# Kernel tuning notes

Hardware: AMD Instinct MI355X
Metric: run time of the kernel (lower is better)

The kernel has to match this reference:

```python
import jax, jax.numpy as jnp
import numpy as np

TEMPERATURE = 0.07
COS_EPS = 1e-8          # torch F.cosine_similarity eps
MASK_FILL = -9e15       # value used to mask the diagonal


def setup_inputs() -> dict:
    key = jax.random.key(0)
    k1, k2 = jax.random.split(key)
    B, D = 4096, 256
    z_i = jax.random.normal(k1, (B, D), dtype=jnp.float32)
    z_j = jax.random.normal(k2, (B, D), dtype=jnp.float32)
    return {"z_i": z_i, "z_j": z_j}


def reference(z_i, z_j):
    B = z_i.shape[0]
    z = jnp.concatenate([z_i, z_j], axis=0)                 # [2B, D]
    # cosine similarity = normalized-GEMM (same math as broadcasted version)
    norms = jnp.maximum(jnp.linalg.norm(z, axis=-1, keepdims=True), COS_EPS)
    zn = z / norms                                          # [2B, D]
    sim = zn @ zn.T                                         # [2B, 2B]
    # fused diagonal mask + temperature scale
    diag = jnp.eye(2 * B, dtype=bool)
    logits = jnp.where(diag, MASK_FILL, sim) / TEMPERATURE  # [2B, 2B]
    # positive pair labels: row k pairs with row (k+B) mod 2B
    labels = jnp.concatenate([jnp.arange(B, 2 * B), jnp.arange(0, B)])
    logp = jax.nn.log_softmax(logits, axis=-1)
    loss = -jnp.mean(jnp.take_along_axis(logp, labels[:, None], axis=-1))
    return loss
```

## Files before the change

### kernel.cpp

```cpp
#include <hip/hip_runtime.h>
#include <hip/hip_bf16.h>

#define B_ROWS 4096
#define TWOB   8192
#define DIM    256
#define INV_T  14.285714285714286f

#define BM 128
#define BN 128
#define NSTRIP 8
#define CT_PER_STRIP 8

typedef __bf16 bf16x8 __attribute__((ext_vector_type(8)));
typedef float  f32x4  __attribute__((ext_vector_type(4)));

__global__ __launch_bounds__(256) void normalize_k(const float* __restrict__ zi,
                                                   const float* __restrict__ zj,
                                                   unsigned short* __restrict__ zn,
                                                   float* __restrict__ loss_acc,
                                                   unsigned int* __restrict__ counter) {
    if (blockIdx.x == 0 && threadIdx.x == 0) {
        loss_acc[0] = 0.0f;
        counter[0]  = 0u;
    }
    int wave = threadIdx.x >> 6;
    int lane = threadIdx.x & 63;
    int row  = blockIdx.x * 4 + wave;
    const float* src = (row < B_ROWS) ? (zi + (size_t)row * DIM)
                                      : (zj + (size_t)(row - B_ROWS) * DIM);
    float4 v = reinterpret_cast<const float4*>(src)[lane];
    float ss = v.x * v.x + v.y * v.y + v.z * v.z + v.w * v.w;
#pragma unroll
    for (int off = 32; off >= 1; off >>= 1) ss += __shfl_xor(ss, off);
    float norm = sqrtf(ss);
    norm = fmaxf(norm, 1e-8f);
    float inv = 1.0f / norm;
    ushort4 o;
    o.x = __builtin_bit_cast(unsigned short, __float2bfloat16(v.x * inv));
    o.y = __builtin_bit_cast(unsigned short, __float2bfloat16(v.y * inv));
    o.z = __builtin_bit_cast(unsigned short, __float2bfloat16(v.z * inv));
    o.w = __builtin_bit_cast(unsigned short, __float2bfloat16(v.w * inv));
    reinterpret_cast<ushort4*>(zn)[(size_t)row * 64 + lane] = o;
}

__global__ __launch_bounds__(256) void ntxent_main(const unsigned short* __restrict__ znu,
                                                   float* __restrict__ pos,
                                                   float* __restrict__ strip_sums) {
    const __bf16* zn = (const __bf16*)znu;
    __shared__ __attribute__((aligned(16))) __bf16 As[8][BM * 32];
    __shared__ __attribute__((aligned(16))) __bf16 Bs[2][BN * 32];

    const int tid  = threadIdx.x;
    const int wave = tid >> 6;
    const int lane = tid & 63;
    const int wr = wave >> 1, wc = wave & 1;
    const int quad = lane >> 4, lc = lane & 15;
    const int rt    = blockIdx.x;
    const int strip = blockIdx.y;
    const int row0  = rt * BM;
    const int posTile = (rt + 32) & 63;

    int stg_off[2];
#pragma unroll
    for (int t = 0; t < 2; ++t) {
        int c  = (wave * 2 + t) * 64 + lane;
        int m  = c >> 2;
        int kc = (c & 3) ^ ((m & 3) ^ ((m >> 2) & 3));
        stg_off[t] = m * DIM + kc * 8;
    }

    const int sw    = (lc & 3) ^ ((lc >> 2) & 3);
    const int aBase = (wr * 64 + lc) * 64 + ((quad ^ sw) * 16);
    const int bBase = (wc * 64 + lc) * 64 + ((quad ^ sw) * 16);

#pragma unroll
    for (int kt = 0; kt < 8; ++kt) {
#pragma unroll
        for (int t = 0; t < 2; ++t) {
            const int j = wave * 2 + t;
            const __bf16* ga = zn + row0 * DIM + kt * 32 + stg_off[t];
            __builtin_amdgcn_global_load_lds(
                (const __attribute__((address_space(1))) void*)ga,
                (__attribute__((address_space(3))) void*)((char*)As + kt * 8192 + j * 1024), 16, 0, 0);
        }
    }
    {
        const int col0 = strip * CT_PER_STRIP * BN;
#pragma unroll
        for (int t = 0; t < 2; ++t) {
            const int j = wave * 2 + t;
            const __bf16* gb = zn + col0 * DIM + stg_off[t];
            __builtin_amdgcn_global_load_lds(
                (const __attribute__((address_space(1))) void*)gb,
                (__attribute__((address_space(3))) void*)((char*)Bs + j * 1024), 16, 0, 0);
        }
    }

    f32x4 acc[4][4];
    float rsum[4][4];
#pragma unroll
    for (int mi = 0; mi < 4; ++mi)
#pragma unroll
        for (int r = 0; r < 4; ++r) rsum[mi][r] = 0.0f;

    for (int ct = 0; ct < CT_PER_STRIP; ++ct) {
        const int colTile = strip * CT_PER_STRIP + ct;
        const int col0 = colTile * BN;
#pragma unroll
        for (int mi = 0; mi < 4; ++mi)
#pragma unroll
            for (int ni = 0; ni < 4; ++ni) acc[mi][ni] = f32x4{0.f, 0.f, 0.f, 0.f};

#pragma unroll
        for (int kt = 0; kt < 8; ++kt) {
            __syncthreads();

            {
                const int nct = (kt == 7) ? ct + 1 : ct;
                const int nkt = (kt + 1) & 7;
                if (nct < CT_PER_STRIP) {
                    const int ncol0 = (strip * CT_PER_STRIP + nct) * BN;
#pragma unroll
                    for (int t = 0; t < 2; ++t) {
                        const int j = wave * 2 + t;
                        const __bf16* gb = zn + ncol0 * DIM + nkt * 32 + stg_off[t];
                        __builtin_amdgcn_global_load_lds(
                            (const __attribute__((address_space(1))) void*)gb,
                            (__attribute__((address_space(3))) void*)((char*)Bs + ((kt + 1) & 1) * 8192 + j * 1024),
                            16, 0, 0);
                    }
                }
            }

            bf16x8 af[4], bfr[4];
#pragma unroll
            for (int mi = 0; mi < 4; ++mi)
                af[mi] = *(const bf16x8*)((const char*)As + kt * 8192 + aBase + mi * 1024);
#pragma unroll
            for (int ni = 0; ni < 4; ++ni)
                bfr[ni] = *(const bf16x8*)((const char*)Bs + (kt & 1) * 8192 + bBase + ni * 1024);
#pragma unroll
            for (int mi = 0; mi < 4; ++mi)
#pragma unroll
                for (int ni = 0; ni < 4; ++ni)
                    acc[mi][ni] = __builtin_amdgcn_mfma_f32_16x16x32_bf16(
                        af[mi], bfr[ni], acc[mi][ni], 0, 0, 0);
        }

        const bool special = (colTile == rt) || (colTile == posTile);
#pragma unroll
        for (int mi = 0; mi < 4; ++mi) {
#pragma unroll
            for (int ni = 0; ni < 4; ++ni) {
                f32x4 a = acc[mi][ni];
#pragma unroll
                for (int r = 0; r < 4; ++r) {
                    float logit = a[r] * INV_T;
                    float e = __expf(logit);
                    if (special) {
                        int gr = row0 + wr * 64 + mi * 16 + quad * 4 + r;
                        int gc = col0 + wc * 64 + ni * 16 + lc;
                        if (gc == ((gr + B_ROWS) & (TWOB - 1))) pos[gr] = logit;
                        if (gr == gc) e = 0.0f;
                    }
                    rsum[mi][r] += e;
                }
            }
        }
    }

    __syncthreads();
    float* rowsumL = (float*)As;
#pragma unroll
    for (int mi = 0; mi < 4; ++mi) {
#pragma unroll
        for (int r = 0; r < 4; ++r) {
            float v = rsum[mi][r];
            v += __shfl_xor(v, 1);
            v += __shfl_xor(v, 2);
            v += __shfl_xor(v, 4);
            v += __shfl_xor(v, 8);
            if (lc == 0) rowsumL[wc * BM + wr * 64 + mi * 16 + quad * 4 + r] = v;
        }
    }
    __syncthreads();
    if (tid < BM)
        strip_sums[(size_t)strip * TWOB + row0 + tid] = rowsumL[tid] + rowsumL[BM + tid];
}

__global__ __launch_bounds__(256) void finalize_k(const float* __restrict__ strip_sums,
                                                  const float* __restrict__ pos,
                                                  float* __restrict__ loss_acc,
                                                  unsigned int* __restrict__ counter,
                                                  float* __restrict__ out) {
    __shared__ float wsums[4];
    const int tid = threadIdx.x;
    const int r   = blockIdx.x * 256 + tid;
    float s = 0.0f;
#pragma unroll
    for (int st = 0; st < NSTRIP; ++st) s += strip_sums[(size_t)st * TWOB + r];
    float local = logf(s) - pos[r];
#pragma unroll
    for (int off = 32; off >= 1; off >>= 1) local += __shfl_xor(local, off);
    if ((tid & 63) == 0) wsums[tid >> 6] = local;
    __syncthreads();
    if (tid == 0) {
        float bsum = wsums[0] + wsums[1] + wsums[2] + wsums[3];
        atomicAdd(loss_acc, bsum);
        __threadfence();
        unsigned int done = atomicAdd(counter, 1u);
        if (done == gridDim.x - 1) {
            float total = atomicAdd(loss_acc, 0.0f);
            out[0] = total / (float)TWOB;
        }
    }
}

extern "C" void kernel_launch(void* const* d_in, const int* in_sizes, int n_in,
                              void* d_out, int out_size, void* d_ws, size_t ws_size,
                              hipStream_t stream) {
    const float* zi = (const float*)d_in[0];
    const float* zj = (const float*)d_in[1];
    unsigned short* zn = (unsigned short*)d_ws;
    float* pos        = (float*)((char*)d_ws + (size_t)TWOB * DIM * 2);
    float* strip_sums = pos + TWOB;
    float* loss_acc   = strip_sums + (size_t)NSTRIP * TWOB;
    unsigned int* counter = (unsigned int*)(loss_acc + 1);
    float* out = (float*)d_out;

    normalize_k<<<dim3(TWOB / 4), 256, 0, stream>>>(zi, zj, zn, loss_acc, counter);
    ntxent_main<<<dim3(64, NSTRIP), 256, 0, stream>>>(zn, pos, strip_sums);
    finalize_k<<<dim3(TWOB / 256), 256, 0, stream>>>(strip_sums, pos, loss_acc, counter, out);
}
```

Measured before the change: 107.1 us.

## Load B fragments directly from global memory, drop LDS double buffer and barriers

The B operand tiles are no longer staged through a double-buffered LDS buffer. Each lane now reads its bf16x8 fragment straight from global memory, relying on L2 and L1 caching since zn is small. This removes the per-k-step __syncthreads and LDS traffic for B. The kernel also asks for 2 blocks per CU via launch bounds, raises wave priority around the MFMA bursts, and stops unrolling the column-tile loop. The cost is exposed global load latency inside the inner loop with no explicit prefetch, plus less-coalesced per-lane 16-byte reads.

```diff
diff --git a/kernel.cpp b/kernel.cpp
--- a/kernel.cpp
+++ b/kernel.cpp
@@ -43,12 +43,11 @@
     reinterpret_cast<ushort4*>(zn)[(size_t)row * 64 + lane] = o;
 }
 
-__global__ __launch_bounds__(256) void ntxent_main(const unsigned short* __restrict__ znu,
-                                                   float* __restrict__ pos,
-                                                   float* __restrict__ strip_sums) {
+__global__ __launch_bounds__(256, 2) void ntxent_main(const unsigned short* __restrict__ znu,
+                                                      float* __restrict__ pos,
+                                                      float* __restrict__ strip_sums) {
     const __bf16* zn = (const __bf16*)znu;
     __shared__ __attribute__((aligned(16))) __bf16 As[8][BM * 32];
-    __shared__ __attribute__((aligned(16))) __bf16 Bs[2][BN * 32];
 
     const int tid  = threadIdx.x;
     const int wave = tid >> 6;
@@ -69,10 +68,6 @@
         stg_off[t] = m * DIM + kc * 8;
     }
 
-    const int sw    = (lc & 3) ^ ((lc >> 2) & 3);
-    const int aBase = (wr * 64 + lc) * 64 + ((quad ^ sw) * 16);
-    const int bBase = (wc * 64 + lc) * 64 + ((quad ^ sw) * 16);
-
 #pragma unroll
     for (int kt = 0; kt < 8; ++kt) {
 #pragma unroll
@@ -84,28 +79,25 @@
                 (__attribute__((address_space(3))) void*)((char*)As + kt * 8192 + j * 1024), 16, 0, 0);
         }
     }
-    {
-        const int col0 = strip * CT_PER_STRIP * BN;
-#pragma unroll
-        for (int t = 0; t < 2; ++t) {
-            const int j = wave * 2 + t;
-            const __bf16* gb = zn + col0 * DIM + stg_off[t];
-            __builtin_amdgcn_global_load_lds(
-                (const __attribute__((address_space(1))) void*)gb,
-                (__attribute__((address_space(3))) void*)((char*)Bs + j * 1024), 16, 0, 0);
-        }
-    }
+
+    const int sw    = (lc & 3) ^ ((lc >> 2) & 3);
+    const int aBase = (wr * 64 + lc) * 64 + ((quad ^ sw) * 16);
+    const char* bRow = (const char*)zn + (size_t)(wc * 64 + lc) * (DIM * 2) + quad * 16;
+
+    float rsum[4][4];
+#pragma unroll
+    for (int mi = 0; mi < 4; ++mi)
+#pragma unroll
+        for (int r = 0; r < 4; ++r) rsum[mi][r] = 0.0f;
+
+    __syncthreads();
 
     f32x4 acc[4][4];
-    float rsum[4][4];
-#pragma unroll
-    for (int mi = 0; mi < 4; ++mi)
-#pragma unroll
-        for (int r = 0; r < 4; ++r) rsum[mi][r] = 0.0f;
-
+#pragma unroll 1
     for (int ct = 0; ct < CT_PER_STRIP; ++ct) {
         const int colTile = strip * CT_PER_STRIP + ct;
         const int col0 = colTile * BN;
+        const char* bp = bRow + (size_t)col0 * (DIM * 2);
 #pragma unroll
         for (int mi = 0; mi < 4; ++mi)
 #pragma unroll
@@ -113,38 +105,21 @@
 
 #pragma unroll
         for (int kt = 0; kt < 8; ++kt) {
-            __syncthreads();
-
-            {
-                const int nct = (kt == 7) ? ct + 1 : ct;
-                const int nkt = (kt + 1) & 7;
-                if (nct < CT_PER_STRIP) {
-                    const int ncol0 = (strip * CT_PER_STRIP + nct) * BN;
-#pragma unroll
-                    for (int t = 0; t < 2; ++t) {
-                        const int j = wave * 2 + t;
-                        const __bf16* gb = zn + ncol0 * DIM + nkt * 32 + stg_off[t];
-                        __builtin_amdgcn_global_load_lds(
-                            (const __attribute__((address_space(1))) void*)gb,
-                            (__attribute__((address_space(3))) void*)((char*)Bs + ((kt + 1) & 1) * 8192 + j * 1024),
-                            16, 0, 0);
-                    }
-                }
-            }
-
             bf16x8 af[4], bfr[4];
+#pragma unroll
+            for (int ni = 0; ni < 4; ++ni)
+                bfr[ni] = *(const bf16x8*)(bp + ni * (16 * DIM * 2) + kt * 64);
 #pragma unroll
             for (int mi = 0; mi < 4; ++mi)
                 af[mi] = *(const bf16x8*)((const char*)As + kt * 8192 + aBase + mi * 1024);
-#pragma unroll
-            for (int ni = 0; ni < 4; ++ni)
-                bfr[ni] = *(const bf16x8*)((const char*)Bs + (kt & 1) * 8192 + bBase + ni * 1024);
+            __builtin_amdgcn_s_setprio(1);
 #pragma unroll
             for (int mi = 0; mi < 4; ++mi)
 #pragma unroll
                 for (int ni = 0; ni < 4; ++ni)
                     acc[mi][ni] = __builtin_amdgcn_mfma_f32_16x16x32_bf16(
                         af[mi], bfr[ni], acc[mi][ni], 0, 0, 0);
+            __builtin_amdgcn_s_setprio(0);
         }
 
         const bool special = (colTile == rt) || (colTile == posTile);
```

Result: slower. 132.5 us (+23.7%).

## Exploit similarity-matrix symmetry to compute only half the tiles

Applied to the files above, without the earlier changes.

Because the similarity matrix is symmetric, each block now computes only the column tiles at circular distances q*4..q*4+3 (plus the distance-32 positive tile for half the row tiles), roughly halving the MFMA and exp work. Each off-diagonal tile contributes both row sums and column sums; column sums are reduced through LDS and written to per-distance slots. The finalize kernel sums 40 partial slots instead of 8. The cost is extra shuffles, syncs, and global writes per tile, plus a larger workspace and more reads in finalize.

```diff
diff --git a/kernel.cpp b/kernel.cpp
--- a/kernel.cpp
+++ b/kernel.cpp
@@ -8,8 +8,8 @@
 
 #define BM 128
 #define BN 128
-#define NSTRIP 8
-#define CT_PER_STRIP 8
+#define NQ 8
+#define NSLOT 41
 
 typedef __bf16 bf16x8 __attribute__((ext_vector_type(8)));
 typedef float  f32x4  __attribute__((ext_vector_type(4)));
@@ -55,10 +55,12 @@
     const int lane = tid & 63;
     const int wr = wave >> 1, wc = wave & 1;
     const int quad = lane >> 4, lc = lane & 15;
-    const int rt    = blockIdx.x;
-    const int strip = blockIdx.y;
-    const int row0  = rt * BM;
-    const int posTile = (rt + 32) & 63;
+    const int rt = blockIdx.x;
+    const int q  = blockIdx.y;
+    const int q4 = q * 4;
+    const int row0 = rt * BM;
+    const int NCT = (q == 7 && rt < 32) ? 5 : 4;
+#define COLOF(i) ((rt + (((i) == 4) ? 32 : (q4 + (i)))) & 63)
 
     int stg_off[2];
 #pragma unroll
@@ -85,7 +87,7 @@
         }
     }
     {
-        const int col0 = strip * CT_PER_STRIP * BN;
+        const int col0 = COLOF(0) * BN;
 #pragma unroll
         for (int t = 0; t < 2; ++t) {
             const int j = wave * 2 + t;
@@ -98,14 +100,17 @@
 
     f32x4 acc[4][4];
     float rsum[4][4];
+    float posv[4] = {0.f, 0.f, 0.f, 0.f};
+    int   posm[4] = {-1, -1, -1, -1};
 #pragma unroll
     for (int mi = 0; mi < 4; ++mi)
 #pragma unroll
         for (int r = 0; r < 4; ++r) rsum[mi][r] = 0.0f;
 
-    for (int ct = 0; ct < CT_PER_STRIP; ++ct) {
-        const int colTile = strip * CT_PER_STRIP + ct;
-        const int col0 = colTile * BN;
+    for (int ct = 0; ct < NCT; ++ct) {
+        const int jdist = (ct == 4) ? 32 : (q4 + ct);
+        const int c     = (rt + jdist) & 63;
+        const int col0  = c * BN;
 #pragma unroll
         for (int mi = 0; mi < 4; ++mi)
 #pragma unroll
@@ -118,8 +123,8 @@
             {
                 const int nct = (kt == 7) ? ct + 1 : ct;
                 const int nkt = (kt + 1) & 7;
-                if (nct < CT_PER_STRIP) {
-                    const int ncol0 = (strip * CT_PER_STRIP + nct) * BN;
+                if (nct < NCT) {
+                    const int ncol0 = COLOF(nct) * BN;
 #pragma unroll
                     for (int t = 0; t < 2; ++t) {
                         const int j = wave * 2 + t;
@@ -147,7 +152,9 @@
                         af[mi], bfr[ni], acc[mi][ni], 0, 0, 0);
         }
 
-        const bool special = (colTile == rt) || (colTile == posTile);
+        const bool isDiag = (jdist == 0);
+        const bool isPos  = (jdist == 32);
+        float cadd[4] = {0.f, 0.f, 0.f, 0.f};
 #pragma unroll
         for (int mi = 0; mi < 4; ++mi) {
 #pragma unroll
@@ -157,17 +164,43 @@
                 for (int r = 0; r < 4; ++r) {
                     float logit = a[r] * INV_T;
                     float e = __expf(logit);
-                    if (special) {
+                    if (isDiag || isPos) {
                         int gr = row0 + wr * 64 + mi * 16 + quad * 4 + r;
                         int gc = col0 + wc * 64 + ni * 16 + lc;
-                        if (gc == ((gr + B_ROWS) & (TWOB - 1))) pos[gr] = logit;
-                        if (gr == gc) e = 0.0f;
+                        if (isPos && gc == gr + B_ROWS) { posv[mi] = logit; posm[mi] = gr; }
+                        if (isDiag && gr == gc) e = 0.0f;
                     }
                     rsum[mi][r] += e;
+                    cadd[ni]    += e;
                 }
             }
         }
-    }
+
+        if (!isDiag) {
+#pragma unroll
+            for (int ni = 0; ni < 4; ++ni) {
+                cadd[ni] += __shfl_xor(cadd[ni], 16);
+                cadd[ni] += __shfl_xor(cadd[ni], 32);
+            }
+            __syncthreads();
+            float* colsumL = (float*)((char*)Bs + 8192);
+            if (quad == 0) {
+#pragma unroll
+                for (int ni = 0; ni < 4; ++ni)
+                    colsumL[wr * 128 + wc * 64 + ni * 16 + lc] = cadd[ni];
+            }
+            __syncthreads();
+            if (tid < BM)
+                strip_sums[(size_t)jdist * TWOB + col0 + tid] = colsumL[tid] + colsumL[BM + tid];
+        }
+    }
+
+#pragma unroll
+    for (int mi = 0; mi < 4; ++mi)
+        if (posm[mi] >= 0) {
+            pos[posm[mi]] = posv[mi];
+            pos[posm[mi] + B_ROWS] = posv[mi];
+        }
 
     __syncthreads();
     float* rowsumL = (float*)As;
@@ -185,7 +218,7 @@
     }
     __syncthreads();
     if (tid < BM)
-        strip_sums[(size_t)strip * TWOB + row0 + tid] = rowsumL[tid] + rowsumL[BM + tid];
+        strip_sums[(size_t)(33 + q) * TWOB + row0 + tid] = rowsumL[tid] + rowsumL[BM + tid];
 }
 
 __global__ __launch_bounds__(256) void finalize_k(const float* __restrict__ strip_sums,
@@ -198,7 +231,10 @@
     const int r   = blockIdx.x * 256 + tid;
     float s = 0.0f;
 #pragma unroll
-    for (int st = 0; st < NSTRIP; ++st) s += strip_sums[(size_t)st * TWOB + r];
+    for (int j = 1; j <= 31; ++j) s += strip_sums[(size_t)j * TWOB + r];
+    if (r >= B_ROWS) s += strip_sums[(size_t)32 * TWOB + r];
+#pragma unroll
+    for (int qq = 0; qq < NQ; ++qq) s += strip_sums[(size_t)(33 + qq) * TWOB + r];
     float local = logf(s) - pos[r];
 #pragma unroll
     for (int off = 32; off >= 1; off >>= 1) local += __shfl_xor(local, off);
@@ -224,11 +260,11 @@
     unsigned short* zn = (unsigned short*)d_ws;
     float* pos        = (float*)((char*)d_ws + (size_t)TWOB * DIM * 2);
     float* strip_sums = pos + TWOB;
-    float* loss_acc   = strip_sums + (size_t)NSTRIP * TWOB;
+    float* loss_acc   = strip_sums + (size_t)NSLOT * TWOB;
     unsigned int* counter = (unsigned int*)(loss_acc + 1);
     float* out = (float*)d_out;
 
     normalize_k<<<dim3(TWOB / 4), 256, 0, stream>>>(zi, zj, zn, loss_acc, counter);
-    ntxent_main<<<dim3(64, NSTRIP), 256, 0, stream>>>(zn, pos, strip_sums);
+    ntxent_main<<<dim3(64, NQ), 256, 0, stream>>>(zn, pos, strip_sums);
     finalize_k<<<dim3(TWOB / 256), 256, 0, stream>>>(strip_sums, pos, loss_acc, counter, out);
 }
```

New measurement: 98.86 us. -7.7%, faster.
